# Kernel tuning notes

Hardware: AMD Instinct MI355X
Metric: run time of the kernel (lower is better)

## Reference

```python
import jax, jax.numpy as jnp
import numpy as np
from jax import lax

T, E, H2, K = 2048, 768, 512, 7
START, STOP = 5, 6
NEG = -10000.0


def setup_inputs() -> dict:
    key = jax.random.key(0)
    ks = jax.random.split(key, 16)
    s = 0.05  # weight init scale
    trans = jax.random.normal(ks[13], (K, K), jnp.float32)
    trans = trans.at[START, :].set(NEG)   # never transition INTO start
    trans = trans.at[:, STOP].set(NEG)    # never transition FROM stop
    return {
        "embeds": jax.random.normal(ks[0], (T, E), jnp.float32),
        "h0": jax.random.normal(ks[1], (2, H2), jnp.float32),
        "c0": jax.random.normal(ks[2], (2, H2), jnp.float32),
        "W_ih_f": jax.random.normal(ks[3], (4 * H2, E), jnp.float32) * s,
        "W_hh_f": jax.random.normal(ks[4], (4 * H2, H2), jnp.float32) * s,
        "b_ih_f": jax.random.normal(ks[5], (4 * H2,), jnp.float32) * s,
        "b_hh_f": jax.random.normal(ks[6], (4 * H2,), jnp.float32) * s,
        "W_ih_b": jax.random.normal(ks[7], (4 * H2, E), jnp.float32) * s,
        "W_hh_b": jax.random.normal(ks[8], (4 * H2, H2), jnp.float32) * s,
        "b_ih_b": jax.random.normal(ks[9], (4 * H2,), jnp.float32) * s,
        "b_hh_b": jax.random.normal(ks[10], (4 * H2,), jnp.float32) * s,
        "W_out": jax.random.normal(ks[11], (K, 1024), jnp.float32) * s,
        "b_out": jax.random.normal(ks[12], (K,), jnp.float32) * s,
        "transitions": trans,
    }


def _lstm_dir(xs, h0, c0, W_ih, W_hh, b_ih, b_hh):
    # xs: [T, E] -> hs: [T, H2]. PyTorch gate order i, f, g, o.
    pre = xs @ W_ih.T + (b_ih + b_hh)  # [T, 4*H2]

    def step(carry, px):
        h, c = carry
        z = px + h @ W_hh.T
        i, f, g, o = jnp.split(z, 4)
        i, f, o = jax.nn.sigmoid(i), jax.nn.sigmoid(f), jax.nn.sigmoid(o)
        c = f * c + i * jnp.tanh(g)
        h = o * jnp.tanh(c)
        return (h, c), h

    _, hs = lax.scan(step, (h0, c0), pre)
    return hs


def _viterbi(feats, transitions):
    # feats: [T, K]. Vectorized over the tag dimension (replaces per-tag loop).
    init = jnp.full((K,), NEG, feats.dtype).at[START].set(0.0)

    def step(fv, feat):
        nv = fv[None, :] + transitions           # [K_next, K_prev]
        bptr = jnp.argmax(nv, axis=1)            # best prev tag per next tag
        fv_new = jnp.max(nv, axis=1) + feat
        return fv_new, bptr

    fv, bptrs = lax.scan(step, init, feats)      # bptrs: [T, K]
    term = fv + transitions[STOP]
    best = jnp.argmax(term)
    path_score = term[best]

    def back(tag, bp):
        return bp[tag], tag                       # emit tag at step t, carry prev

    _, path = lax.scan(back, best, bptrs, reverse=True)  # path: [T] int
    return path_score, path


def reference(embeds, h0, c0, W_ih_f, W_hh_f, b_ih_f, b_hh_f,
              W_ih_b, W_hh_b, b_ih_b, b_hh_b, W_out, b_out, transitions):
    # BiLSTM over the (SciBERT-contextualized) embeddings, batch=1
    hs_f = _lstm_dir(embeds, h0[0], c0[0], W_ih_f, W_hh_f, b_ih_f, b_hh_f)
    hs_b = _lstm_dir(embeds[::-1], h0[1], c0[1], W_ih_b, W_hh_b, b_ih_b, b_hh_b)[::-1]
    lstm_out = jnp.concatenate([hs_f, hs_b], axis=-1)   # [T, hidden_dim]
    feats = lstm_out @ W_out.T + b_out                   # [T, K]
    path_score, best_path = _viterbi(feats, transitions)
    return path_score, best_path
```

## Files before the change

### kernel.cpp

```cpp
#include <hip/hip_runtime.h>

#define TT 2048
#define EE 768
#define HH 512
#define GG 2048
#define KK 7
#define NEGV -10000.0f
#define TAG_START 5
#define TAG_STOP 6

__device__ __forceinline__ float sigf(float x) { return 1.0f / (1.0f + __expf(-x)); }
__device__ __forceinline__ float tanh_f(float x) { return 1.0f - 2.0f / (__expf(2.0f * x) + 1.0f); }

__global__ __launch_bounds__(256) void gemm_pre(
    const float* __restrict__ embeds,
    const float* __restrict__ Wf, const float* __restrict__ bif, const float* __restrict__ bhf,
    const float* __restrict__ Wb, const float* __restrict__ bib, const float* __restrict__ bhb,
    float* __restrict__ pre_f, float* __restrict__ pre_b)
{
    const int dir = blockIdx.z;
    const float* __restrict__ W  = dir ? Wb  : Wf;
    const float* __restrict__ bi = dir ? bib : bif;
    const float* __restrict__ bh = dir ? bhb : bhf;
    float* __restrict__ out = dir ? pre_b : pre_f;
    const int n0 = blockIdx.x * 128;
    const int m0 = blockIdx.y * 128;
    __shared__ __align__(16) float As[16][128];
    __shared__ __align__(16) float Bs[16][128];
    const int tid  = threadIdx.x;
    const int lrow = tid >> 1;
    const int lch  = tid & 1;
    const int tx = tid & 15, ty = tid >> 4;
    float acc[8][8];
    #pragma unroll
    for (int i = 0; i < 8; ++i)
        #pragma unroll
        for (int j = 0; j < 8; ++j) acc[i][j] = 0.0f;

    for (int k0 = 0; k0 < EE; k0 += 16) {
        const int am   = m0 + lrow;
        const int arow = dir ? (TT - 1 - am) : am;
        const float4* ap = (const float4*)(embeds + (size_t)arow * EE + k0 + lch * 8);
        const float4 a0 = ap[0], a1 = ap[1];
        const float4* bp = (const float4*)(W + (size_t)(n0 + lrow) * EE + k0 + lch * 8);
        const float4 b0 = bp[0], b1 = bp[1];
        __syncthreads();
        As[lch*8+0][lrow]=a0.x; As[lch*8+1][lrow]=a0.y; As[lch*8+2][lrow]=a0.z; As[lch*8+3][lrow]=a0.w;
        As[lch*8+4][lrow]=a1.x; As[lch*8+5][lrow]=a1.y; As[lch*8+6][lrow]=a1.z; As[lch*8+7][lrow]=a1.w;
        Bs[lch*8+0][lrow]=b0.x; Bs[lch*8+1][lrow]=b0.y; Bs[lch*8+2][lrow]=b0.z; Bs[lch*8+3][lrow]=b0.w;
        Bs[lch*8+4][lrow]=b1.x; Bs[lch*8+5][lrow]=b1.y; Bs[lch*8+6][lrow]=b1.z; Bs[lch*8+7][lrow]=b1.w;
        __syncthreads();
        #pragma unroll
        for (int k = 0; k < 16; ++k) {
            const float4 xa0 = *(const float4*)&As[k][ty*8];
            const float4 xa1 = *(const float4*)&As[k][ty*8+4];
            const float4 xb0 = *(const float4*)&Bs[k][tx*8];
            const float4 xb1 = *(const float4*)&Bs[k][tx*8+4];
            const float av[8] = {xa0.x,xa0.y,xa0.z,xa0.w,xa1.x,xa1.y,xa1.z,xa1.w};
            const float bv[8] = {xb0.x,xb0.y,xb0.z,xb0.w,xb1.x,xb1.y,xb1.z,xb1.w};
            #pragma unroll
            for (int i = 0; i < 8; ++i)
                #pragma unroll
                for (int j = 0; j < 8; ++j)
                    acc[i][j] = fmaf(av[i], bv[j], acc[i][j]);
        }
    }
    float bb[8];
    #pragma unroll
    for (int j = 0; j < 8; ++j) { const int n = n0 + tx*8 + j; bb[j] = bi[n] + bh[n]; }
    #pragma unroll
    for (int i = 0; i < 8; ++i) {
        const int m = m0 + ty*8 + i;
        float4 o0, o1;
        o0.x=acc[i][0]+bb[0]; o0.y=acc[i][1]+bb[1]; o0.z=acc[i][2]+bb[2]; o0.w=acc[i][3]+bb[3];
        o1.x=acc[i][4]+bb[4]; o1.y=acc[i][5]+bb[5]; o1.z=acc[i][6]+bb[6]; o1.w=acc[i][7]+bb[7];
        float4* op = (float4*)(out + (size_t)m * GG + n0 + tx*8);
        op[0] = o0; op[1] = o1;
    }
}

__global__ __launch_bounds__(512, 2) void lstm_scan(
    const float* __restrict__ Whh_f, const float* __restrict__ Whh_b,
    const float* __restrict__ h0, const float* __restrict__ c0,
    const float* __restrict__ pre_f, const float* __restrict__ pre_b,
    float* __restrict__ hs_f, float* __restrict__ hs_b,
    float* __restrict__ hbuf, int* __restrict__ cnt)
{
    const int bx = blockIdx.x;
    const int d = bx >> 4;
    const int w = bx & 15;
    const float* __restrict__ Whh = d ? Whh_b : Whh_f;
    const float* __restrict__ pre = d ? pre_b : pre_f;
    float* __restrict__ hs = d ? hs_b : hs_f;
    float* __restrict__ hb = hbuf + d * 2 * HH;
    int* cn = cnt + (size_t)d * TT * 32;
    const int tid = threadIdx.x;
    const int v = tid >> 6;
    const int l = tid & 63;

    float wreg[16][8];
    #pragma unroll
    for (int r = 0; r < 16; ++r) {
        const int rho = v * 16 + r;
        const int R = (rho >> 5) * HH + w * 32 + (rho & 31);
        const float4* src = (const float4*)(Whh + (size_t)R * HH + l * 8);
        const float4 w0 = src[0], w1 = src[1];
        wreg[r][0]=w0.x; wreg[r][1]=w0.y; wreg[r][2]=w0.z; wreg[r][3]=w0.w;
        wreg[r][4]=w1.x; wreg[r][5]=w1.y; wreg[r][6]=w1.z; wreg[r][7]=w1.w;
    }
    const bool comb = (v == 0) && (l < 32);
    float creg = comb ? c0[d * HH + w * 32 + l] : 0.0f;
    float hreg[8];
    {
        const float4* hp = (const float4*)(h0 + d * HH + l * 8);
        const float4 ha = hp[0], hc = hp[1];
        hreg[0]=ha.x; hreg[1]=ha.y; hreg[2]=ha.z; hreg[3]=ha.w;
        hreg[4]=hc.x; hreg[5]=hc.y; hreg[6]=hc.z; hreg[7]=hc.w;
    }
    __shared__ float zsum[128];
    const int Rl = ((l & 1) << 3) | ((l & 2) << 1) | ((l & 4) >> 1) | ((l & 8) >> 3);
    long long budget = 50000000LL;

    for (int s = 0; s < TT; ++s) {
        float pg0 = 0.f, pg1 = 0.f, pg2 = 0.f, pg3 = 0.f;
        if (comb) {
            const float* pp = pre + (size_t)s * GG + w * 32 + l;
            pg0 = pp[0]; pg1 = pp[HH]; pg2 = pp[2*HH]; pg3 = pp[3*HH];
        }
        if (s > 0) {
            if (tid == 0) {
                while (__hip_atomic_load(cn + (size_t)(s - 1) * 32, __ATOMIC_ACQUIRE,
                                         __HIP_MEMORY_SCOPE_AGENT) < 16) {
                    if (--budget < 0) break;
                    __builtin_amdgcn_s_sleep(1);
                }
            }
            __syncthreads();
            const float4* hp = (const float4*)(hb + (s & 1) * HH + l * 8);
            const float4 ha = hp[0], hc = hp[1];
            hreg[0]=ha.x; hreg[1]=ha.y; hreg[2]=ha.z; hreg[3]=ha.w;
            hreg[4]=hc.x; hreg[5]=hc.y; hreg[6]=hc.z; hreg[7]=hc.w;
        }
        float acc[16];
        #pragma unroll
        for (int r = 0; r < 16; ++r) {
            float a = wreg[r][0] * hreg[0];
            #pragma unroll
            for (int i = 1; i < 8; ++i) a = fmaf(wreg[r][i], hreg[i], a);
            acc[r] = a;
        }
        #pragma unroll
        for (int r = 0; r < 16; ++r) acc[r] += __shfl_xor(acc[r], 1);
        float t8[8];
        #pragma unroll
        for (int r = 0; r < 8; ++r) t8[r] = (l & 1) ? acc[8 + r] : acc[r];
        #pragma unroll
        for (int r = 0; r < 8; ++r) t8[r] += __shfl_xor(t8[r], 2);
        float t4[4];
        #pragma unroll
        for (int r = 0; r < 4; ++r) t4[r] = (l & 2) ? t8[4 + r] : t8[r];
        #pragma unroll
        for (int r = 0; r < 4; ++r) t4[r] += __shfl_xor(t4[r], 4);
        float t2[2];
        #pragma unroll
        for (int r = 0; r < 2; ++r) t2[r] = (l & 4) ? t4[2 + r] : t4[r];
        #pragma unroll
        for (int r = 0; r < 2; ++r) t2[r] += __shfl_xor(t2[r], 8);
        float val = (l & 8) ? t2[1] : t2[0];
        val += __shfl_xor(val, 16);
        val += __shfl_xor(val, 32);
        if (l < 16) zsum[v * 16 + Rl] = val;
        __syncthreads();
        if (comb) {
            const float zi = zsum[l]      + pg0;
            const float zf = zsum[32 + l] + pg1;
            const float zg = zsum[64 + l] + pg2;
            const float zo = zsum[96 + l] + pg3;
            const float ig = sigf(zi), fg = sigf(zf), gg = tanh_f(zg), og = sigf(zo);
            creg = fg * creg + ig * gg;
            const float hn = og * tanh_f(creg);
            hb[((s + 1) & 1) * HH + w * 32 + l] = hn;
            hs[(size_t)s * HH + w * 32 + l] = hn;
        }
        if (tid == 0) {
            __hip_atomic_fetch_add(cn + (size_t)s * 32, 1, __ATOMIC_RELEASE,
                                   __HIP_MEMORY_SCOPE_AGENT);
        }
    }
}

__global__ __launch_bounds__(256) void feats_k(
    const float* __restrict__ hsf, const float* __restrict__ hsb,
    const float* __restrict__ Wout, const float* __restrict__ bout,
    float* __restrict__ feats)
{
    const int wv = threadIdx.x >> 6;
    const int l  = threadIdx.x & 63;
    const int t  = blockIdx.x * 4 + wv;
    float acc[KK];
    #pragma unroll
    for (int k = 0; k < KK; ++k) acc[k] = 0.0f;
    const float* hf  = hsf + (size_t)t * HH;
    const float* hbp = hsb + (size_t)(TT - 1 - t) * HH;
    for (int c = l; c < HH; c += 64) {
        const float xf = hf[c];
        const float xb = hbp[c];
        #pragma unroll
        for (int k = 0; k < KK; ++k)
            acc[k] += xf * Wout[k * 1024 + c] + xb * Wout[k * 1024 + HH + c];
    }
    #pragma unroll
    for (int k = 0; k < KK; ++k) {
        #pragma unroll
        for (int m = 1; m <= 32; m <<= 1) acc[k] += __shfl_xor(acc[k], m);
    }
    if (l == 0) {
        #pragma unroll
        for (int k = 0; k < KK; ++k) feats[t * KK + k] = acc[k] + bout[k];
    }
}

__global__ __launch_bounds__(64) void viterbi_k(
    const float* __restrict__ feats, const float* __restrict__ trans,
    float* __restrict__ out)
{
    __shared__ float fl[TT * KK];
    __shared__ unsigned char bp[TT * KK];
    __shared__ unsigned char path[TT];
    const int l = threadIdx.x;
    for (int i = l; i < TT * KK; i += 64) fl[i] = feats[i];
    const int kn = l >> 3, kp = l & 7;
    const float tr = (kn < 7 && kp < 7) ? trans[kn * 7 + kp] : -1e30f;
    float fv = (kp == 7) ? -1e30f : ((kp == TAG_START) ? 0.0f : NEGV);
    const int srcl = (l & 7) << 3;
    __syncthreads();
    for (int t = 0; t < TT; ++t) {
        float vv = fv + tr;
        int bi = kp;
        #pragma unroll
        for (int m = 1; m <= 4; m <<= 1) {
            const float ov = __shfl_xor(vv, m);
            const int   oi = __shfl_xor(bi, m);
            if (ov > vv || (ov == vv && oi < bi)) { vv = ov; bi = oi; }
        }
        const float feat = fl[t * KK + (kn < 7 ? kn : 6)];
        const float fvn = vv + feat;
        if (kp == 0 && kn < 7) bp[t * KK + kn] = (unsigned char)bi;
        fv = __shfl(fvn, srcl);
        if ((l & 7) == 7) fv = -1e30f;
    }
    float tv = (l < 7) ? (fv + trans[TAG_STOP * 7 + l]) : -1e30f;
    int ti = l & 7;
    #pragma unroll
    for (int m = 1; m <= 4; m <<= 1) {
        const float ov = __shfl_xor(tv, m);
        const int   oi = __shfl_xor(ti, m);
        if (ov > tv || (ov == tv && oi < ti)) { tv = ov; ti = oi; }
    }
    __syncthreads();
    if (l == 0) {
        out[0] = tv;
        int tag = ti;
        path[TT - 1] = (unsigned char)tag;
        for (int t = TT - 1; t >= 1; --t) {
            tag = bp[t * KK + tag];
            path[t - 1] = (unsigned char)tag;
        }
    }
    __syncthreads();
    for (int t = l; t < TT; t += 64) out[1 + t] = (float)path[t];
}

extern "C" void kernel_launch(void* const* d_in, const int* in_sizes, int n_in,
                              void* d_out, int out_size, void* d_ws, size_t ws_size,
                              hipStream_t stream) {
    const float* embeds = (const float*)d_in[0];
    const float* h0     = (const float*)d_in[1];
    const float* c0     = (const float*)d_in[2];
    const float* Wihf   = (const float*)d_in[3];
    const float* Whhf   = (const float*)d_in[4];
    const float* bihf   = (const float*)d_in[5];
    const float* bhhf   = (const float*)d_in[6];
    const float* Wihb   = (const float*)d_in[7];
    const float* Whhb   = (const float*)d_in[8];
    const float* bihb   = (const float*)d_in[9];
    const float* bhhb   = (const float*)d_in[10];
    const float* Wout   = (const float*)d_in[11];
    const float* bout   = (const float*)d_in[12];
    const float* trans  = (const float*)d_in[13];
    float* out = (float*)d_out;

    float* ws    = (float*)d_ws;
    float* pre_f = ws;
    float* pre_b = pre_f + (size_t)TT * GG;
    float* hs_f  = pre_b + (size_t)TT * GG;
    float* hs_b  = hs_f + (size_t)TT * HH;
    float* feats = hs_b + (size_t)TT * HH;
    float* hbuf  = feats + (size_t)TT * KK;
    int*   cnt   = (int*)(hbuf + 4 * HH);

    hipMemsetAsync(cnt, 0, (size_t)2 * TT * 32 * sizeof(int), stream);
    gemm_pre<<<dim3(16, 16, 2), 256, 0, stream>>>(
        embeds, Wihf, bihf, bhhf, Wihb, bihb, bhhb, pre_f, pre_b);
    lstm_scan<<<32, 512, 0, stream>>>(
        Whhf, Whhb, h0, c0, pre_f, pre_b, hs_f, hs_b, hbuf, cnt);
    feats_k<<<TT / 4, 256, 0, stream>>>(hs_f, hs_b, Wout, bout, feats);
    viterbi_k<<<1, 64, 0, stream>>>(feats, trans, out);
}
```

Baseline: 10.15 ms.

## Store recurrent LSTM weights as bf16 in LDS instead of registers

Moves each block's slice of W_hh out of 128 fp32 registers per thread into shared memory, rounded to bf16 (128x512 shorts = 128KB), and unpacks it to fp32 on every step. The aim is to cut register pressure and drop the launch_bounds min-blocks hint. The cost is an LDS read of the weights on every timestep and lower precision in the recurrent matvec, which can change the argmax path in the Viterbi decode.

```diff
diff --git a/kernel.cpp b/kernel.cpp
--- a/kernel.cpp
+++ b/kernel.cpp
@@ -79,7 +79,7 @@
     }
 }
 
-__global__ __launch_bounds__(512, 2) void lstm_scan(
+__global__ __launch_bounds__(512) void lstm_scan(
     const float* __restrict__ Whh_f, const float* __restrict__ Whh_b,
     const float* __restrict__ h0, const float* __restrict__ c0,
     const float* __restrict__ pre_f, const float* __restrict__ pre_b,
@@ -98,16 +98,28 @@
     const int v = tid >> 6;
     const int l = tid & 63;
 
-    float wreg[16][8];
-    #pragma unroll
-    for (int r = 0; r < 16; ++r) {
-        const int rho = v * 16 + r;
+    __shared__ __align__(16) unsigned short wlds[128][512];
+    __shared__ float zsum[128];
+
+    for (int i = tid; i < 128 * 128; i += 512) {
+        const int rho = i >> 7;
+        const int c4  = i & 127;
         const int R = (rho >> 5) * HH + w * 32 + (rho & 31);
-        const float4* src = (const float4*)(Whh + (size_t)R * HH + l * 8);
-        const float4 w0 = src[0], w1 = src[1];
-        wreg[r][0]=w0.x; wreg[r][1]=w0.y; wreg[r][2]=w0.z; wreg[r][3]=w0.w;
-        wreg[r][4]=w1.x; wreg[r][5]=w1.y; wreg[r][6]=w1.z; wreg[r][7]=w1.w;
-    }
+        const float4 wv = *(const float4*)(Whh + (size_t)R * HH + c4 * 4);
+        const unsigned int b0 = __float_as_uint(wv.x);
+        const unsigned int b1 = __float_as_uint(wv.y);
+        const unsigned int b2 = __float_as_uint(wv.z);
+        const unsigned int b3 = __float_as_uint(wv.w);
+        const unsigned int r0 = (b0 + 0x7FFFu + ((b0 >> 16) & 1u)) >> 16;
+        const unsigned int r1 = (b1 + 0x7FFFu + ((b1 >> 16) & 1u)) >> 16;
+        const unsigned int r2 = (b2 + 0x7FFFu + ((b2 >> 16) & 1u)) >> 16;
+        const unsigned int r3 = (b3 + 0x7FFFu + ((b3 >> 16) & 1u)) >> 16;
+        uint2 pk;
+        pk.x = r0 | (r1 << 16);
+        pk.y = r2 | (r3 << 16);
+        *(uint2*)&wlds[rho][c4 * 4] = pk;
+    }
+
     const bool comb = (v == 0) && (l < 32);
     float creg = comb ? c0[d * HH + w * 32 + l] : 0.0f;
     float hreg[8];
@@ -117,9 +129,9 @@
         hreg[0]=ha.x; hreg[1]=ha.y; hreg[2]=ha.z; hreg[3]=ha.w;
         hreg[4]=hc.x; hreg[5]=hc.y; hreg[6]=hc.z; hreg[7]=hc.w;
     }
-    __shared__ float zsum[128];
     const int Rl = ((l & 1) << 3) | ((l & 2) << 1) | ((l & 4) >> 1) | ((l & 8) >> 3);
     long long budget = 50000000LL;
+    __syncthreads();
 
     for (int s = 0; s < TT; ++s) {
         float pg0 = 0.f, pg1 = 0.f, pg2 = 0.f, pg3 = 0.f;
@@ -144,9 +156,17 @@
         float acc[16];
         #pragma unroll
         for (int r = 0; r < 16; ++r) {
-            float a = wreg[r][0] * hreg[0];
-            #pragma unroll
-            for (int i = 1; i < 8; ++i) a = fmaf(wreg[r][i], hreg[i], a);
+            const int rho = v * 16 + r;
+            const uint4 q = *(const uint4*)&wlds[rho][l * 8];
+            float a;
+            a  = __uint_as_float(q.x << 16)         * hreg[0];
+            a  = fmaf(__uint_as_float(q.x & 0xFFFF0000u), hreg[1], a);
+            a  = fmaf(__uint_as_float(q.y << 16),         hreg[2], a);
+            a  = fmaf(__uint_as_float(q.y & 0xFFFF0000u), hreg[3], a);
+            a  = fmaf(__uint_as_float(q.z << 16),         hreg[4], a);
+            a  = fmaf(__uint_as_float(q.z & 0xFFFF0000u), hreg[5], a);
+            a  = fmaf(__uint_as_float(q.w << 16),         hreg[6], a);
+            a  = fmaf(__uint_as_float(q.w & 0xFFFF0000u), hreg[7], a);
             acc[r] = a;
         }
         #pragma unroll
```

Result: no change. 10.01 ms (-1.4%).
